# Optimization experiments

Measured on AMD Instinct MI355X. Metric: run time of the kernel, lower is better.

Reference implementation:

```python
import jax, jax.numpy as jnp
import numpy as np

B = 8                                   # point clouds per batch
NS = [65536, 16384, 4096, 1024, 256]    # points per scale (stride-4 downsampling)
CS = [32, 64, 128, 256, 512]            # encoder channels per scale
K = 3
BN_EPS = 1e-5


def setup_inputs() -> dict:
    key = jax.random.key(0)
    ks = iter(jax.random.split(key, 64))
    inp = {}
    for i, (n, c) in enumerate(zip(NS, CS)):
        inp[f"p{i}"] = jax.random.uniform(next(ks), (n, 3), jnp.float32)
        inp[f"f{i}"] = jax.random.normal(next(ks), (n, c), jnp.float32)
        inp[f"b{i}"] = jnp.repeat(jnp.arange(B, dtype=jnp.int32), n // B)
    # FP stage mlps: a:(4->3) [768,256,256], b:(3->2) [384,128,128],
    #               c:(2->1) [192,64,64],   d:(1->0) [96,32,32]
    cfg = {"a": (CS[3] + CS[4], CS[3]), "b": (CS[2] + CS[3], CS[2]),
           "c": (CS[1] + CS[2], CS[1]), "d": (CS[0] + CS[1], CS[0])}
    for s, (cin, ch) in cfg.items():
        for j, ci in ((1, cin), (2, ch)):
            inp[f"w{s}{j}"] = jax.random.normal(next(ks), (ci, ch), jnp.float32) / float(np.sqrt(ci))
            inp[f"bias{s}{j}"] = jnp.zeros((ch,), jnp.float32)
            inp[f"g{s}{j}"] = jnp.ones((ch,), jnp.float32)
            inp[f"bt{s}{j}"] = jnp.zeros((ch,), jnp.float32)
    return inp


def _knn_interpolate(x2, p2, p1):
    """torch_geometric.nn.knn_interpolate with k=3; equal-sized sorted batches."""
    n1, n2, c = p1.shape[0] // B, p2.shape[0] // B, x2.shape[1]
    p1b, p2b = p1.reshape(B, n1, 3), p2.reshape(B, n2, 3)
    x2b = x2.reshape(B, n2, c)
    # squared dists via |a|^2 + |b|^2 - 2ab (avoids [B,n1,n2,3] temporary)
    d2 = (jnp.sum(p1b * p1b, -1)[:, :, None] + jnp.sum(p2b * p2b, -1)[:, None, :]
          - 2.0 * jnp.einsum('bnd,bmd->bnm', p1b, p2b))
    neg_d2, idx = jax.lax.top_k(-d2, K)              # [B, n1, K]
    w = 1.0 / jnp.maximum(-neg_d2, 1e-16)            # inverse squared distance
    gath = jax.vmap(lambda x, i: x[i])(x2b, idx)     # [B, n1, K, c]
    out = jnp.einsum('bnk,bnkc->bnc', w, gath) / jnp.sum(w, -1, keepdims=True)
    return out.reshape(B * n1, c)


def _lin_bn_relu(x, w, bias, gamma, beta):
    h = x @ w + bias
    mu = jnp.mean(h, 0)
    var = jnp.mean((h - mu) ** 2, 0)
    return jax.nn.relu((h - mu) * jax.lax.rsqrt(var + BN_EPS) * gamma + beta)


def _fp_stage(p_fine, f_fine, p_coarse, f_coarse, w1, b1, g1, bt1, w2, b2, g2, bt2):
    up = _knn_interpolate(f_coarse, p_coarse, p_fine)
    x = jnp.concatenate([f_fine, up], axis=1)
    x = _lin_bn_relu(x, w1, b1, g1, bt1)
    return _lin_bn_relu(x, w2, b2, g2, bt2)


def reference(p0, p1, p2, p3, p4, f0, f1, f2, f3, f4, b0, b1, b2, b3, b4,
              wa1, biasa1, ga1, bta1, wa2, biasa2, ga2, bta2,
              wb1, biasb1, gb1, btb1, wb2, biasb2, gb2, btb2,
              wc1, biasc1, gc1, btc1, wc2, biasc2, gc2, btc2,
              wd1, biasd1, gd1, btd1, wd2, biasd2, gd2, btd2):
    f3 = _fp_stage(p3, f3, p4, f4, wa1, biasa1, ga1, bta1, wa2, biasa2, ga2, bta2)
    f2 = _fp_stage(p2, f2, p3, f3, wb1, biasb1, gb1, btb1, wb2, biasb2, gb2, btb2)
    f1 = _fp_stage(p1, f1, p2, f2, wc1, biasc1, gc1, btc1, wc2, biasc2, gc2, btc2)
    f0 = _fp_stage(p0, f0, p1, f1, wd1, biasd1, gd1, btd1, wd2, biasd2, gd2, btd2)
    return f0
```

## Files before the change

### kernel.cpp

```cpp
#include <hip/hip_runtime.h>

#define BN_EPS 1e-5f

typedef unsigned short us;

__device__ __forceinline__ float bf2f(us u) {
    union { unsigned int i; float f; } v; v.i = ((unsigned int)u) << 16; return v.f;
}
__device__ __forceinline__ us f2bf(float f) {
    unsigned int x = __float_as_uint(f);
    x += 0x7fffu + ((x >> 16) & 1u);
    return (us)(x >> 16);
}
__device__ __forceinline__ float ldf(const void* p, size_t i, int f32) {
    return f32 ? ((const float*)p)[i] : bf2f(((const us*)p)[i]);
}

__global__ void detect_kernel(const unsigned int* __restrict__ g, int* __restrict__ flag) {
    if (threadIdx.x == 0 && blockIdx.x == 0)
        *flag = ((g[0] & 0xFFFFu) == 0u) ? 1 : 0;
}

template<int MODE, int FPB, int SPLIT, int N2>
__global__ __launch_bounds__(FPB * SPLIT)
void knn_up_kernel(
    const void* __restrict__ p_fine,
    const void* __restrict__ p_coarse,
    const void* __restrict__ f_coarse,
    const float* __restrict__ stats,
    const void* __restrict__ gamma,
    const void* __restrict__ beta,
    float inv_n2,
    float* __restrict__ up_out,
    const int* __restrict__ pf32,
    int n2pb, int c2)
{
    __shared__ __align__(16) float cpx[N2], cpy[N2], cpz[N2], cs2[N2];
    __shared__ float aff_a[256], aff_b[256];
    __shared__ float cand_d[FPB][3 * SPLIT];
    __shared__ int   cand_i[FPB][3 * SPLIT];
    __shared__ int   s_idx[FPB][3];
    __shared__ float s_w[FPB][3];

    const int f32 = *pf32;
    const int tid = threadIdx.x;
    const int cbase = blockIdx.y * n2pb;

    for (int j = tid; j < n2pb; j += FPB * SPLIT) {
        const size_t b = (size_t)(cbase + j) * 3;
        const float x = ldf(p_coarse, b + 0, f32);
        const float y = ldf(p_coarse, b + 1, f32);
        const float z = ldf(p_coarse, b + 2, f32);
        cpx[j] = x; cpy[j] = y; cpz[j] = z;
        cs2[j] = __fadd_rn(__fadd_rn(__fmul_rn(x, x), __fmul_rn(y, y)), __fmul_rn(z, z));
    }
    if (MODE == 1) {
        for (int c = tid; c < c2; c += FPB * SPLIT) {
            float mu  = stats[c] * inv_n2;
            float var = stats[c2 + c] * inv_n2 - mu * mu;
            float a = ldf(gamma, c, f32) * rsqrtf(var + BN_EPS);
            aff_a[c] = a;
            aff_b[c] = ldf(beta, c, f32) - mu * a;
        }
    }
    __syncthreads();

    {
        const int f = tid % FPB;
        const int s = tid / FPB;
        const int row = (blockIdx.y * gridDim.x + blockIdx.x) * FPB + f;
        const size_t b = (size_t)row * 3;
        const float px = ldf(p_fine, b + 0, f32);
        const float py = ldf(p_fine, b + 1, f32);
        const float pz = ldf(p_fine, b + 2, f32);
        const float s1 = __fadd_rn(__fadd_rn(__fmul_rn(px, px), __fmul_rn(py, py)),
                                   __fmul_rn(pz, pz));
        const int len = n2pb / SPLIT;
        const int jb = s * len;
        float t0 = 1e30f, t1 = 1e30f, t2 = 1e30f;
        int i0 = jb, i1 = jb, i2 = jb;
        for (int j = jb; j < jb + len; j += 4) {
            const float4 X = *(const float4*)&cpx[j];
            const float4 Y = *(const float4*)&cpy[j];
            const float4 Z = *(const float4*)&cpz[j];
            const float4 S = *(const float4*)&cs2[j];
            #pragma unroll
            for (int q = 0; q < 4; ++q) {
                const float qx = ((const float*)&X)[q];
                const float qy = ((const float*)&Y)[q];
                const float qz = ((const float*)&Z)[q];
                const float s2 = ((const float*)&S)[q];
                const float dot = fmaf(pz, qz, fmaf(py, qy, __fmul_rn(px, qx)));
                const float d = __fsub_rn(__fadd_rn(s1, s2), __fmul_rn(2.0f, dot));
                const int jj = j + q;
                const bool a0 = d < t0, a1 = d < t1, a2 = d < t2;
                t2 = a1 ? t1 : (a2 ? d : t2);  i2 = a1 ? i1 : (a2 ? jj : i2);
                t1 = a0 ? t0 : (a1 ? d : t1);  i1 = a0 ? i0 : (a1 ? jj : i1);
                t0 = a0 ? d  : t0;             i0 = a0 ? jj : i0;
            }
        }
        cand_d[f][s * 3 + 0] = t0;  cand_i[f][s * 3 + 0] = cbase + i0;
        cand_d[f][s * 3 + 1] = t1;  cand_i[f][s * 3 + 1] = cbase + i1;
        cand_d[f][s * 3 + 2] = t2;  cand_i[f][s * 3 + 2] = cbase + i2;
    }
    __syncthreads();

    if (tid < FPB) {
        const int f = tid;
        unsigned used = 0;
        #pragma unroll
        for (int k = 0; k < 3; ++k) {
            float bd = 1e38f; int bi = 0x7fffffff; int bq = 0;
            for (int q = 0; q < 3 * SPLIT; ++q) {
                if (used & (1u << q)) continue;
                const float d = cand_d[f][q]; const int i = cand_i[f][q];
                if (d < bd || (d == bd && i < bi)) { bd = d; bi = i; bq = q; }
            }
            used |= 1u << bq;
            s_idx[f][k] = bi;
            s_w[f][k] = __fdiv_rn(1.0f, fmaxf(bd, 1e-16f));
        }
    }
    __syncthreads();

    const int lane = tid & 63, wv = tid >> 6;
    const int nw = (FPB * SPLIT) / 64;
    for (int p = wv; p < FPB; p += nw) {
        const int row = (blockIdx.y * gridDim.x + blockIdx.x) * FPB + p;
        const int g0 = s_idx[p][0], g1 = s_idx[p][1], g2 = s_idx[p][2];
        const float w0 = s_w[p][0], w1 = s_w[p][1], w2 = s_w[p][2];
        const float den = __fadd_rn(__fadd_rn(w0, w1), w2);
        float* __restrict__ urow = up_out + (size_t)row * c2;
        for (int c = lane; c < c2; c += 64) {
            float v0, v1, v2;
            if (MODE == 0) {
                v0 = ldf(f_coarse, (size_t)g0 * c2 + c, f32);
                v1 = ldf(f_coarse, (size_t)g1 * c2 + c, f32);
                v2 = ldf(f_coarse, (size_t)g2 * c2 + c, f32);
            } else {
                const float* fc = (const float*)f_coarse;
                const float aa = aff_a[c], bb = aff_b[c];
                v0 = fmaxf(aa * fc[(size_t)g0 * c2 + c] + bb, 0.f);
                v1 = fmaxf(aa * fc[(size_t)g1 * c2 + c] + bb, 0.f);
                v2 = fmaxf(aa * fc[(size_t)g2 * c2 + c] + bb, 0.f);
            }
            const float num = fmaf(w2, v2, fmaf(w1, v1, __fmul_rn(w0, v0)));
            urow[c] = __fdiv_rn(num, den);
        }
    }
}

__global__ __launch_bounds__(256)
void gemm1_bn_kernel(const void* __restrict__ Ffine,
                     const float* __restrict__ Up,
                     const void* __restrict__ W,
                     const void* __restrict__ bias,
                     float* __restrict__ H,
                     float* __restrict__ stats_out,
                     const int* __restrict__ pf32,
                     int M, int c1, int c2, int N)
{
    __shared__ __align__(16) float As[16][68];
    __shared__ __align__(16) float Bs[16][68];
    __shared__ float s_sum[64], s_sq[64];

    const int f32 = *pf32;
    const int K = c1 + c2;
    const int tid = threadIdx.x;
    const int tx = tid & 15, ty = tid >> 4;
    const int n0 = blockIdx.x * 64, m0 = blockIdx.y * 64;

    if (tid < 64) { s_sum[tid] = 0.f; s_sq[tid] = 0.f; }
    __syncthreads();

    const int a_m = tid >> 2;
    const int a_k = (tid & 3) << 2;
    const int b_k = tid >> 4;
    const int b_n = (tid & 15) << 2;

    float acc[4][4] = {};

    for (int k0 = 0; k0 < K; k0 += 16) {
        const int k = k0 + a_k;
        const int row = m0 + a_m;
        float av[4];
        if (k < c1) {
            if (f32) {
                const float4 v = *(const float4*)((const float*)Ffine + (size_t)row * c1 + k);
                av[0] = v.x; av[1] = v.y; av[2] = v.z; av[3] = v.w;
            } else {
                const ushort4 u = *(const ushort4*)((const us*)Ffine + (size_t)row * c1 + k);
                av[0] = bf2f(u.x); av[1] = bf2f(u.y); av[2] = bf2f(u.z); av[3] = bf2f(u.w);
            }
        } else {
            const float4 v = *(const float4*)(Up + (size_t)row * c2 + (k - c1));
            av[0] = v.x; av[1] = v.y; av[2] = v.z; av[3] = v.w;
        }
        #pragma unroll
        for (int i = 0; i < 4; ++i) As[a_k + i][a_m] = av[i];

        float4 bv = make_float4(0.f, 0.f, 0.f, 0.f);
        if (n0 + b_n < N) {
            const size_t wi = (size_t)(k0 + b_k) * N + (n0 + b_n);
            if (f32) {
                bv = *(const float4*)((const float*)W + wi);
            } else {
                const ushort4 u = *(const ushort4*)((const us*)W + wi);
                bv = make_float4(bf2f(u.x), bf2f(u.y), bf2f(u.z), bf2f(u.w));
            }
        }
        *(float4*)&Bs[b_k][b_n] = bv;

        __syncthreads();
        #pragma unroll
        for (int kk = 0; kk < 16; ++kk) {
            const float4 a4 = *(const float4*)&As[kk][ty << 2];
            const float4 b4 = *(const float4*)&Bs[kk][tx << 2];
            const float aarr[4] = {a4.x, a4.y, a4.z, a4.w};
            const float barr[4] = {b4.x, b4.y, b4.z, b4.w};
            #pragma unroll
            for (int i = 0; i < 4; ++i)
                #pragma unroll
                for (int j = 0; j < 4; ++j)
                    acc[i][j] = fmaf(aarr[i], barr[j], acc[i][j]);
        }
        __syncthreads();
    }

    float bvals[4];
    const bool colsok = (n0 + (tx << 2)) < N;
    #pragma unroll
    for (int j = 0; j < 4; ++j) {
        const int n = n0 + (tx << 2) + j;
        bvals[j] = (n < N) ? ldf(bias, n, f32) : 0.f;
    }
    float ps[4] = {0.f, 0.f, 0.f, 0.f}, pq[4] = {0.f, 0.f, 0.f, 0.f};
    #pragma unroll
    for (int i = 0; i < 4; ++i) {
        float4 hv;
        float* hvp = (float*)&hv;
        #pragma unroll
        for (int j = 0; j < 4; ++j) {
            const float v = acc[i][j] + bvals[j];
            hvp[j] = v;
            ps[j] += v;
            pq[j] = fmaf(v, v, pq[j]);
        }
        if (colsok)
            *(float4*)(H + (size_t)(m0 + (ty << 2) + i) * N + n0 + (tx << 2)) = hv;
    }
    #pragma unroll
    for (int j = 0; j < 4; ++j) {
        atomicAdd(&s_sum[(tx << 2) + j], ps[j]);
        atomicAdd(&s_sq[(tx << 2) + j], pq[j]);
    }
    __syncthreads();
    if (tid < 64) {
        const int n = n0 + tid;
        if (n < N) {
            atomicAdd(&stats_out[n], s_sum[tid]);
            atomicAdd(&stats_out[N + n], s_sq[tid]);
        }
    }
}

__global__ __launch_bounds__(256)
void gemm2_bn_kernel(const float* __restrict__ A,
                     const void* __restrict__ W,
                     const void* __restrict__ bias,
                     const float* __restrict__ stats_in,
                     const void* __restrict__ g_in,
                     const void* __restrict__ bt_in,
                     float inv_m,
                     float* __restrict__ H,
                     float* __restrict__ stats_out,
                     const int* __restrict__ pf32,
                     int M, int K, int N)
{
    __shared__ __align__(16) float As[16][68];
    __shared__ __align__(16) float Bs[16][68];
    __shared__ float aff_a[256], aff_b[256];
    __shared__ float s_sum[64], s_sq[64];

    const int f32 = *pf32;
    const int tid = threadIdx.x;
    const int tx = tid & 15, ty = tid >> 4;
    const int n0 = blockIdx.x * 64, m0 = blockIdx.y * 64;

    for (int c = tid; c < K; c += 256) {
        float mu  = stats_in[c] * inv_m;
        float var = stats_in[K + c] * inv_m - mu * mu;
        float a = ldf(g_in, c, f32) * rsqrtf(var + BN_EPS);
        aff_a[c] = a; aff_b[c] = ldf(bt_in, c, f32) - mu * a;
    }
    if (tid < 64) { s_sum[tid] = 0.f; s_sq[tid] = 0.f; }
    __syncthreads();

    const int a_m = tid >> 2;
    const int a_k = (tid & 3) << 2;
    const int b_k = tid >> 4;
    const int b_n = (tid & 15) << 2;

    float acc[4][4] = {};

    for (int k0 = 0; k0 < K; k0 += 16) {
        const float4 af = *(const float4*)(A + (size_t)(m0 + a_m) * K + (k0 + a_k));
        float av[4] = {af.x, af.y, af.z, af.w};
        #pragma unroll
        for (int i = 0; i < 4; ++i)
            av[i] = fmaxf(fmaf(aff_a[k0 + a_k + i], av[i], aff_b[k0 + a_k + i]), 0.f);
        #pragma unroll
        for (int i = 0; i < 4; ++i) As[a_k + i][a_m] = av[i];

        float4 bv = make_float4(0.f, 0.f, 0.f, 0.f);
        if (n0 + b_n < N) {
            const size_t wi = (size_t)(k0 + b_k) * N + (n0 + b_n);
            if (f32) {
                bv = *(const float4*)((const float*)W + wi);
            } else {
                const ushort4 u = *(const ushort4*)((const us*)W + wi);
                bv = make_float4(bf2f(u.x), bf2f(u.y), bf2f(u.z), bf2f(u.w));
            }
        }
        *(float4*)&Bs[b_k][b_n] = bv;

        __syncthreads();
        #pragma unroll
        for (int kk = 0; kk < 16; ++kk) {
            const float4 a4 = *(const float4*)&As[kk][ty << 2];
            const float4 b4 = *(const float4*)&Bs[kk][tx << 2];
            const float aarr[4] = {a4.x, a4.y, a4.z, a4.w};
            const float barr[4] = {b4.x, b4.y, b4.z, b4.w};
            #pragma unroll
            for (int i = 0; i < 4; ++i)
                #pragma unroll
                for (int j = 0; j < 4; ++j)
                    acc[i][j] = fmaf(aarr[i], barr[j], acc[i][j]);
        }
        __syncthreads();
    }

    float bvals[4];
    const bool colsok = (n0 + (tx << 2)) < N;
    #pragma unroll
    for (int j = 0; j < 4; ++j) {
        const int n = n0 + (tx << 2) + j;
        bvals[j] = (n < N) ? ldf(bias, n, f32) : 0.f;
    }
    float ps[4] = {0.f, 0.f, 0.f, 0.f}, pq[4] = {0.f, 0.f, 0.f, 0.f};
    #pragma unroll
    for (int i = 0; i < 4; ++i) {
        float4 hv;
        float* hvp = (float*)&hv;
        #pragma unroll
        for (int j = 0; j < 4; ++j) {
            const float v = acc[i][j] + bvals[j];
            hvp[j] = v;
            ps[j] += v;
            pq[j] = fmaf(v, v, pq[j]);
        }
        if (colsok)
            *(float4*)(H + (size_t)(m0 + (ty << 2) + i) * N + n0 + (tx << 2)) = hv;
    }
    #pragma unroll
    for (int j = 0; j < 4; ++j) {
        atomicAdd(&s_sum[(tx << 2) + j], ps[j]);
        atomicAdd(&s_sq[(tx << 2) + j], pq[j]);
    }
    __syncthreads();
    if (tid < 64) {
        const int n = n0 + tid;
        if (n < N) {
            atomicAdd(&stats_out[n], s_sum[tid]);
            atomicAdd(&stats_out[N + n], s_sq[tid]);
        }
    }
}

__global__ __launch_bounds__(256)
void finalize_kernel(const float* __restrict__ Hf, const float* __restrict__ stats,
                     const void* __restrict__ g, const void* __restrict__ bt,
                     float inv_m, void* __restrict__ out,
                     const int* __restrict__ pf32, int total)
{
    const int idx = blockIdx.x * 256 + threadIdx.x;
    if (idx >= total) return;
    const int f32 = *pf32;
    const int c = idx & 31;
    const float mu  = stats[c] * inv_m;
    const float var = stats[32 + c] * inv_m - mu * mu;
    const float a = ldf(g, c, f32) * rsqrtf(var + BN_EPS);
    const float b = ldf(bt, c, f32) - mu * a;
    const float v = fmaxf(fmaf(a, Hf[idx], b), 0.f);
    if (f32) ((float*)out)[idx] = v;
    else     ((us*)out)[idx] = f2bf(v);
}

extern "C" void kernel_launch(void* const* d_in, const int* in_sizes, int n_in,
                              void* d_out, int out_size, void* d_ws, size_t ws_size,
                              hipStream_t stream) {
    (void)in_sizes; (void)n_in; (void)out_size; (void)ws_size;
    const void* p0 = d_in[0];
    const void* f0 = d_in[1];
    const void* p1 = d_in[3];
    const void* f1 = d_in[4];
    const void* p2 = d_in[6];
    const void* f2 = d_in[7];
    const void* p3 = d_in[9];
    const void* f3 = d_in[10];
    const void* p4 = d_in[12];
    const void* f4 = d_in[13];
    const void *W1[4], *B1[4], *G1[4], *T1[4], *W2[4], *B2[4], *G2[4], *T2[4];
    for (int s = 0; s < 4; ++s) {
        const int b = 15 + s * 8;
        W1[s] = d_in[b + 0]; B1[s] = d_in[b + 1];
        G1[s] = d_in[b + 2]; T1[s] = d_in[b + 3];
        W2[s] = d_in[b + 4]; B2[s] = d_in[b + 5];
        G2[s] = d_in[b + 6]; T2[s] = d_in[b + 7];
    }

    float* stats = (float*)d_ws;
    float* st_a1 = stats + 0;
    float* st_a2 = stats + 512;
    float* st_b1 = stats + 1024;
    float* st_b2 = stats + 1280;
    float* st_c1 = stats + 1536;
    float* st_c2 = stats + 1664;
    float* st_d1 = stats + 1792;
    float* st_d2 = stats + 1856;
    int*   flag  = (int*)(stats + 1920);
    float* U = (float*)((char*)d_ws + 8192);
    float* H = U + 4194304;
    float* h2a = H + 262144;
    float* h2b = H + 524288;
    float* h2c = H + 1048576;
    float* h2d = U;

    hipMemsetAsync(d_ws, 0, 1920 * sizeof(float), stream);
    detect_kernel<<<1, 64, 0, stream>>>((const unsigned int*)G1[0], flag);

    knn_up_kernel<0, 64, 4, 32><<<dim3(2, 8), 256, 0, stream>>>(
        p3, p4, f4, nullptr, nullptr, nullptr, 0.f, U, flag, 32, 512);
    gemm1_bn_kernel<<<dim3(4, 16), 256, 0, stream>>>(
        f3, U, W1[0], B1[0], H, st_a1, flag, 1024, 256, 512, 256);
    gemm2_bn_kernel<<<dim3(4, 16), 256, 0, stream>>>(
        H, W2[0], B2[0], st_a1, G1[0], T1[0], 1.f / 1024.f,
        h2a, st_a2, flag, 1024, 256, 256);
    knn_up_kernel<1, 64, 4, 128><<<dim3(8, 8), 256, 0, stream>>>(
        p2, p3, h2a, st_a2, G2[0], T2[0], 1.f / 1024.f, U, flag, 128, 256);
    gemm1_bn_kernel<<<dim3(2, 64), 256, 0, stream>>>(
        f2, U, W1[1], B1[1], H, st_b1, flag, 4096, 128, 256, 128);
    gemm2_bn_kernel<<<dim3(2, 64), 256, 0, stream>>>(
        H, W2[1], B2[1], st_b1, G1[1], T1[1], 1.f / 4096.f,
        h2b, st_b2, flag, 4096, 128, 128);
    knn_up_kernel<1, 32, 8, 512><<<dim3(64, 8), 256, 0, stream>>>(
        p1, p2, h2b, st_b2, G2[1], T2[1], 1.f / 4096.f, U, flag, 512, 128);
    gemm1_bn_kernel<<<dim3(1, 256), 256, 0, stream>>>(
        f1, U, W1[2], B1[2], H, st_c1, flag, 16384, 64, 128, 64);
    gemm2_bn_kernel<<<dim3(1, 256), 256, 0, stream>>>(
        H, W2[2], B2[2], st_c1, G1[2], T1[2], 1.f / 16384.f,
        h2c, st_c2, flag, 16384, 64, 64);
    knn_up_kernel<1, 32, 8, 2048><<<dim3(256, 8), 256, 0, stream>>>(
        p0, p1, h2c, st_c2, G2[2], T2[2], 1.f / 16384.f, U, flag, 2048, 64);
    gemm1_bn_kernel<<<dim3(1, 1024), 256, 0, stream>>>(
        f0, U, W1[3], B1[3], H, st_d1, flag, 65536, 32, 64, 32);
    gemm2_bn_kernel<<<dim3(1, 1024), 256, 0, stream>>>(
        H, W2[3], B2[3], st_d1, G1[3], T1[3], 1.f / 65536.f,
        h2d, st_d2, flag, 65536, 32, 32);
    finalize_kernel<<<(65536 * 32) / 256, 256, 0, stream>>>(
        h2d, st_d2, G2[3], T2[3], 1.f / 65536.f, d_out, flag, 65536 * 32);
}
```

Baseline: 583.5 us.

## Prefetch next GEMM tiles into registers and retune KNN split configurations

Both fused GEMM+BN kernels now load the next K-slice of A and W into registers while the current shared-memory tile is being consumed. This software pipelining hides global load latency behind the FMA loop, at the cost of extra registers. The KNN kernels for the two largest stages get larger blocks: one doubles the split count and the other doubles points per block. The candidate-used bitmask is widened to 64 bits so 3*SPLIT candidates fit.

Result: faster. 543.1 us (-6.9%).

```diff
diff --git a/kernel.cpp b/kernel.cpp
--- a/kernel.cpp
+++ b/kernel.cpp
@@ -107,16 +107,16 @@
 
     if (tid < FPB) {
         const int f = tid;
-        unsigned used = 0;
+        unsigned long long used = 0;
         #pragma unroll
         for (int k = 0; k < 3; ++k) {
             float bd = 1e38f; int bi = 0x7fffffff; int bq = 0;
             for (int q = 0; q < 3 * SPLIT; ++q) {
-                if (used & (1u << q)) continue;
+                if (used & (1ull << q)) continue;
                 const float d = cand_d[f][q]; const int i = cand_i[f][q];
                 if (d < bd || (d == bd && i < bi)) { bd = d; bi = i; bq = q; }
             }
-            used |= 1u << bq;
+            used |= 1ull << bq;
             s_idx[f][k] = bi;
             s_w[f][k] = __fdiv_rn(1.0f, fmaxf(bd, 1e-16f));
         }
@@ -171,47 +171,74 @@
     const int n0 = blockIdx.x * 64, m0 = blockIdx.y * 64;
 
     if (tid < 64) { s_sum[tid] = 0.f; s_sq[tid] = 0.f; }
-    __syncthreads();
 
     const int a_m = tid >> 2;
     const int a_k = (tid & 3) << 2;
     const int b_k = tid >> 4;
     const int b_n = (tid & 15) << 2;
-
-    float acc[4][4] = {};
-
-    for (int k0 = 0; k0 < K; k0 += 16) {
-        const int k = k0 + a_k;
-        const int row = m0 + a_m;
-        float av[4];
+    const int row = m0 + a_m;
+
+    float avp[4]; float4 bvp;
+    {
+        const int k = a_k;
         if (k < c1) {
             if (f32) {
                 const float4 v = *(const float4*)((const float*)Ffine + (size_t)row * c1 + k);
-                av[0] = v.x; av[1] = v.y; av[2] = v.z; av[3] = v.w;
+                avp[0] = v.x; avp[1] = v.y; avp[2] = v.z; avp[3] = v.w;
             } else {
                 const ushort4 u = *(const ushort4*)((const us*)Ffine + (size_t)row * c1 + k);
-                av[0] = bf2f(u.x); av[1] = bf2f(u.y); av[2] = bf2f(u.z); av[3] = bf2f(u.w);
+                avp[0] = bf2f(u.x); avp[1] = bf2f(u.y); avp[2] = bf2f(u.z); avp[3] = bf2f(u.w);
             }
         } else {
             const float4 v = *(const float4*)(Up + (size_t)row * c2 + (k - c1));
-            av[0] = v.x; av[1] = v.y; av[2] = v.z; av[3] = v.w;
-        }
-        #pragma unroll
-        for (int i = 0; i < 4; ++i) As[a_k + i][a_m] = av[i];
-
-        float4 bv = make_float4(0.f, 0.f, 0.f, 0.f);
+            avp[0] = v.x; avp[1] = v.y; avp[2] = v.z; avp[3] = v.w;
+        }
+        bvp = make_float4(0.f, 0.f, 0.f, 0.f);
         if (n0 + b_n < N) {
-            const size_t wi = (size_t)(k0 + b_k) * N + (n0 + b_n);
-            if (f32) {
-                bv = *(const float4*)((const float*)W + wi);
+            const size_t wi = (size_t)b_k * N + (n0 + b_n);
+            if (f32) bvp = *(const float4*)((const float*)W + wi);
+            else {
+                const ushort4 u = *(const ushort4*)((const us*)W + wi);
+                bvp = make_float4(bf2f(u.x), bf2f(u.y), bf2f(u.z), bf2f(u.w));
+            }
+        }
+    }
+
+    float acc[4][4] = {};
+
+    for (int k0 = 0; k0 < K; k0 += 16) {
+        #pragma unroll
+        for (int i = 0; i < 4; ++i) As[a_k + i][a_m] = avp[i];
+        *(float4*)&Bs[b_k][b_n] = bvp;
+        __syncthreads();
+
+        float avn[4]; float4 bvn;
+        const int kn = k0 + 16;
+        if (kn < K) {
+            const int k = kn + a_k;
+            if (k < c1) {
+                if (f32) {
+                    const float4 v = *(const float4*)((const float*)Ffine + (size_t)row * c1 + k);
+                    avn[0] = v.x; avn[1] = v.y; avn[2] = v.z; avn[3] = v.w;
+                } else {
+                    const ushort4 u = *(const ushort4*)((const us*)Ffine + (size_t)row * c1 + k);
+                    avn[0] = bf2f(u.x); avn[1] = bf2f(u.y); avn[2] = bf2f(u.z); avn[3] = bf2f(u.w);
+                }
             } else {
-                const ushort4 u = *(const ushort4*)((const us*)W + wi);
-                bv = make_float4(bf2f(u.x), bf2f(u.y), bf2f(u.z), bf2f(u.w));
-            }
-        }
-        *(float4*)&Bs[b_k][b_n] = bv;
-
-        __syncthreads();
+                const float4 v = *(const float4*)(Up + (size_t)row * c2 + (k - c1));
+                avn[0] = v.x; avn[1] = v.y; avn[2] = v.z; avn[3] = v.w;
+            }
+            bvn = make_float4(0.f, 0.f, 0.f, 0.f);
+            if (n0 + b_n < N) {
+                const size_t wi = (size_t)(kn + b_k) * N + (n0 + b_n);
+                if (f32) bvn = *(const float4*)((const float*)W + wi);
+                else {
+                    const ushort4 u = *(const ushort4*)((const us*)W + wi);
+                    bvn = make_float4(bf2f(u.x), bf2f(u.y), bf2f(u.z), bf2f(u.w));
+                }
+            }
+        }
+
         #pragma unroll
         for (int kk = 0; kk < 16; ++kk) {
             const float4 a4 = *(const float4*)&As[kk][ty << 2];
@@ -225,6 +252,12 @@
                     acc[i][j] = fmaf(aarr[i], barr[j], acc[i][j]);
         }
         __syncthreads();
+
+        if (kn < K) {
+            #pragma unroll
+            for (int i = 0; i < 4; ++i) avp[i] = avn[i];
+            bvp = bvn;
+        }
     }
 
     float bvals[4];
@@ -300,31 +333,48 @@
     const int a_k = (tid & 3) << 2;
     const int b_k = tid >> 4;
     const int b_n = (tid & 15) << 2;
+    const int row = m0 + a_m;
+
+    float avp[4]; float4 bvp;
+    {
+        const float4 af = *(const float4*)(A + (size_t)row * K + a_k);
+        avp[0] = af.x; avp[1] = af.y; avp[2] = af.z; avp[3] = af.w;
+        bvp = make_float4(0.f, 0.f, 0.f, 0.f);
+        if (n0 + b_n < N) {
+            const size_t wi = (size_t)b_k * N + (n0 + b_n);
+            if (f32) bvp = *(const float4*)((const float*)W + wi);
+            else {
+                const ushort4 u = *(const ushort4*)((const us*)W + wi);
+                bvp = make_float4(bf2f(u.x), bf2f(u.y), bf2f(u.z), bf2f(u.w));
+            }
+        }
+    }
 
     float acc[4][4] = {};
 
     for (int k0 = 0; k0 < K; k0 += 16) {
-        const float4 af = *(const float4*)(A + (size_t)(m0 + a_m) * K + (k0 + a_k));
-        float av[4] = {af.x, af.y, af.z, af.w};
         #pragma unroll
         for (int i = 0; i < 4; ++i)
-            av[i] = fmaxf(fmaf(aff_a[k0 + a_k + i], av[i], aff_b[k0 + a_k + i]), 0.f);
-        #pragma unroll
-        for (int i = 0; i < 4; ++i) As[a_k + i][a_m] = av[i];
-
-        float4 bv = make_float4(0.f, 0.f, 0.f, 0.f);
-        if (n0 + b_n < N) {
-            const size_t wi = (size_t)(k0 + b_k) * N + (n0 + b_n);
-            if (f32) {
-                bv = *(const float4*)((const float*)W + wi);
-            } else {
-                const ushort4 u = *(const ushort4*)((const us*)W + wi);
-                bv = make_float4(bf2f(u.x), bf2f(u.y), bf2f(u.z), bf2f(u.w));
-            }
-        }
-        *(float4*)&Bs[b_k][b_n] = bv;
-
+            As[a_k + i][a_m] = fmaxf(fmaf(aff_a[k0 + a_k + i], avp[i], aff_b[k0 + a_k + i]), 0.f);
+        *(float4*)&Bs[b_k][b_n] = bvp;
         __syncthreads();
+
+        float avn[4]; float4 bvn;
+        const int kn = k0 + 16;
+        if (kn < K) {
+            const float4 af = *(const float4*)(A + (size_t)row * K + (kn + a_k));
+            avn[0] = af.x; avn[1] = af.y; avn[2] = af.z; avn[3] = af.w;
+            bvn = make_float4(0.f, 0.f, 0.f, 0.f);
+            if (n0 + b_n < N) {
+                const size_t wi = (size_t)(kn + b_k) * N + (n0 + b_n);
+                if (f32) bvn = *(const float4*)((const float*)W + wi);
+                else {
+                    const ushort4 u = *(const ushort4*)((const us*)W + wi);
+                    bvn = make_float4(bf2f(u.x), bf2f(u.y), bf2f(u.z), bf2f(u.w));
+                }
+            }
+        }
+
         #pragma unroll
         for (int kk = 0; kk < 16; ++kk) {
             const float4 a4 = *(const float4*)&As[kk][ty << 2];
@@ -338,6 +388,12 @@
                     acc[i][j] = fmaf(aarr[i], barr[j], acc[i][j]);
         }
         __syncthreads();
+
+        if (kn < K) {
+            #pragma unroll
+            for (int i = 0; i < 4; ++i) avp[i] = avn[i];
+            bvp = bvn;
+        }
     }
 
     float bvals[4];
@@ -453,14 +509,14 @@
     gemm2_bn_kernel<<<dim3(2, 64), 256, 0, stream>>>(
         H, W2[1], B2[1], st_b1, G1[1], T1[1], 1.f / 4096.f,
         h2b, st_b2, flag, 4096, 128, 128);
-    knn_up_kernel<1, 32, 8, 512><<<dim3(64, 8), 256, 0, stream>>>(
+    knn_up_kernel<1, 32, 16, 512><<<dim3(64, 8), 512, 0, stream>>>(
         p1, p2, h2b, st_b2, G2[1], T2[1], 1.f / 4096.f, U, flag, 512, 128);
     gemm1_bn_kernel<<<dim3(1, 256), 256, 0, stream>>>(
         f1, U, W1[2], B1[2], H, st_c1, flag, 16384, 64, 128, 64);
     gemm2_bn_kernel<<<dim3(1, 256), 256, 0, stream>>>(
         H, W2[2], B2[2], st_c1, G1[2], T1[2], 1.f / 16384.f,
         h2c, st_c2, flag, 16384, 64, 64);
-    knn_up_kernel<1, 32, 8, 2048><<<dim3(256, 8), 256, 0, stream>>>(
+    knn_up_kernel<1, 64, 8, 2048><<<dim3(128, 8), 512, 0, stream>>>(
         p0, p1, h2c, st_c2, G2[2], T2[2], 1.f / 16384.f, U, flag, 2048, 64);
     gemm1_bn_kernel<<<dim3(1, 1024), 256, 0, stream>>>(
         f0, U, W1[3], B1[3], H, st_d1, flag, 65536, 32, 64, 32);
```
